# Optimization experiments

Hardware: AMD Instinct MI355X
Metric: run time of the kernel (lower is better)

Reference implementation:

```python
import jax, jax.numpy as jnp
import numpy as np

EPS_F = 1e-12
M, N = 64, 4096  # feature dim m, num nodes n


def setup_inputs() -> dict:
    key = jax.random.key(0)
    k1, k2, k3, k4 = jax.random.split(key, 4)
    # X: (m, n) node features transposed, as in the repo (features.t())
    X = jax.random.normal(k1, (M, N), dtype=jnp.float32)
    # F: (m, m) parameter, xavier_uniform init
    bound = float(np.sqrt(6.0 / (M + M)))
    F = jax.random.uniform(k2, (M, M), minval=-bound, maxval=bound, dtype=jnp.float32)
    # Q_S: (n, n) orthogonal eigenvector matrix of the (symmetric, normalized) adjacency
    A = jax.random.normal(k3, (N, N), dtype=jnp.float32)
    Q_S, _ = jnp.linalg.qr(A)
    Q_S = Q_S.astype(jnp.float32)
    # Lambda_S: (n, 1) eigenvalues of normalized adjacency, inside (-1, 1)
    Lambda_S = jnp.sort(
        jax.random.uniform(k4, (N, 1), minval=-0.95, maxval=0.95, dtype=jnp.float32), axis=0
    )
    gamma = jnp.asarray(0.8, dtype=jnp.float32)
    return {"X": X, "F": F, "Q_S": Q_S, "Lambda_S": Lambda_S, "gamma": gamma}


def reference(X, F, Q_S, Lambda_S, gamma):
    # g(F) = F^T F / (||F^T F||_F + eps)  -- Frobenius-normalized Gram matrix
    FF = F.T @ F                                   # (m, m)
    G_F = FF / (jnp.linalg.norm(FF) + EPS_F)       # (m, m), symmetric PSD, ||.||_F ~ 1
    # spectral decomposition of g(F)
    Lambda_F, Q_F = jnp.linalg.eigh(G_F)           # (m,), (m, m)
    # closed-form equilibrium of Z = gamma * g(F) Z S^T + X in the joint eigenbasis
    D = 1.0 / (1.0 - gamma * Lambda_F[:, None] * Lambda_S.reshape(1, -1))  # (m, n)
    Z = Q_F @ (D * (Q_F.T @ X @ Q_S)) @ Q_S.T      # (m, n)
    return Z
```

## Files before the change

### kernel.cpp

```cpp
#include <hip/hip_runtime.h>
#include <math.h>


typedef short short8 __attribute__((ext_vector_type(8)));
typedef float floatx16 __attribute__((ext_vector_type(16)));

#define KSPLIT 8
#define KCHUNK 512
constexpr int Mdim = 64;
constexpr int Ndim = 4096;

__device__ inline ushort f2bf(float f) {
    uint u = __float_as_uint(f);
    u += 0x7fff + ((u >> 16) & 1);
    return (ushort)(u >> 16);
}
__device__ inline float bf2f(ushort h) { return __uint_as_float(((uint)h) << 16); }

__device__ inline floatx16 mfma_bf16(short8 a, short8 b, floatx16 c) {
    return __builtin_amdgcn_mfma_f32_32x32x16_bf16(a, b, c, 0, 0, 0);
}

struct SharedGemm { ushort Ah[4096], Al[4096], Bh[4096], Bl[4096]; };
struct SharedPrep { float Fraw[64 * 65]; ushort Ph[4096], Pl[4096]; float red[256]; };
union SharedU { SharedGemm g; SharedPrep p; };

__global__ __launch_bounds__(256) void init_kernel(float* __restrict__ W, float* __restrict__ Z) {
    const int i = blockIdx.x * 256 + threadIdx.x;
    float4 z = {0.f, 0.f, 0.f, 0.f};
    if (i < 65536) *(float4*)&W[i * 4] = z;
    else *(float4*)&Z[(i - 65536) * 4] = z;
}

__device__ void prep_body(SharedPrep& sp, const float* __restrict__ F, float* __restrict__ Gout) {
    const int t = threadIdx.x;
    const int l = t & 63, w = t >> 6;
    const int tm = w & 1, tn = w >> 1;
    const int am = tm * 32 + (l & 31);
    const int bn = tn * 32 + (l & 31);
    const int lk = l >> 5;

    for (int s = 0; s < 4; ++s) {
        int e = t + 256 * s;
        int r = e >> 4, q = (e & 15) * 4;
        float4 v = *(const float4*)&F[r * 64 + q];
        float fa[4] = {v.x, v.y, v.z, v.w};
        for (int i = 0; i < 4; ++i) sp.Fraw[r * 65 + q + i] = fa[i];
    }
    __syncthreads();
    {
        int c = t >> 2, kbase = (t & 3) * 16;
        ushort hh[16], ll[16];
#pragma unroll
        for (int kk = 0; kk < 16; ++kk) {
            float v = sp.Fraw[(kbase + kk) * 65 + c];
            ushort h = f2bf(v);
            hh[kk] = h;
            ll[kk] = f2bf(v - bf2f(h));
        }
#pragma unroll
        for (int g = 0; g < 2; ++g) {
            int gk = (kbase >> 3) + g;
            int idx = c * 64 + ((gk ^ (c & 7)) * 8);
#pragma unroll
            for (int u = 0; u < 8; ++u) { sp.Ph[idx + u] = hh[8 * g + u]; sp.Pl[idx + u] = ll[8 * g + u]; }
        }
    }
    __syncthreads();
    floatx16 acc;
    for (int i = 0; i < 16; ++i) acc[i] = 0.f;
    for (int s16 = 0; s16 < 4; ++s16) {
        int gk = 2 * s16 + lk;
        int ai = am * 64 + ((gk ^ (am & 7)) * 8);
        int bi = bn * 64 + ((gk ^ (bn & 7)) * 8);
        short8 ah = *(const short8*)&sp.Ph[ai];
        short8 al = *(const short8*)&sp.Pl[ai];
        short8 bh = *(const short8*)&sp.Ph[bi];
        short8 bl = *(const short8*)&sp.Pl[bi];
        acc = mfma_bf16(ah, bh, acc);
        acc = mfma_bf16(al, bh, acc);
        acc = mfma_bf16(ah, bl, acc);
    }
    float ss = 0.f;
    for (int r = 0; r < 16; ++r) ss += acc[r] * acc[r];
    sp.red[t] = ss;
    __syncthreads();
    for (int off = 128; off > 0; off >>= 1) {
        if (t < off) sp.red[t] += sp.red[t + off];
        __syncthreads();
    }
    const float inv = 1.0f / (sqrtf(sp.red[0]) + 1e-12f);
    for (int r = 0; r < 16; ++r) {
        int row = (r & 3) + 8 * (r >> 2) + 4 * lk + tm * 32;
        int col = tn * 32 + (l & 31);
        float v = acc[r] * inv;
        Gout[row * 64 + col] = v;
        ushort h = f2bf(v);
        int idx = row * 64 + (((col >> 3) ^ (row & 7)) * 8 + (col & 7));
        sp.Ph[idx] = h;
        sp.Pl[idx] = f2bf(v - bf2f(h));
    }
    for (int j = 1; j < 5; ++j) {
        __syncthreads();
        floatx16 a2;
        for (int i = 0; i < 16; ++i) a2[i] = 0.f;
        for (int s16 = 0; s16 < 4; ++s16) {
            int gk = 2 * s16 + lk;
            int ai = am * 64 + ((gk ^ (am & 7)) * 8);
            int bi = bn * 64 + ((gk ^ (bn & 7)) * 8);
            short8 ah = *(const short8*)&sp.Ph[ai];
            short8 al = *(const short8*)&sp.Pl[ai];
            short8 bh = *(const short8*)&sp.Ph[bi];
            short8 bl = *(const short8*)&sp.Pl[bi];
            a2 = mfma_bf16(ah, bh, a2);
            a2 = mfma_bf16(al, bh, a2);
            a2 = mfma_bf16(ah, bl, a2);
        }
        __syncthreads();
        for (int r = 0; r < 16; ++r) {
            int row = (r & 3) + 8 * (r >> 2) + 4 * lk + tm * 32;
            int col = tn * 32 + (l & 31);
            float v = a2[r];
            Gout[j * 4096 + row * 64 + col] = v;
            ushort h = f2bf(v);
            int idx = row * 64 + (((col >> 3) ^ (row & 7)) * 8 + (col & 7));
            sp.Ph[idx] = h;
            sp.Pl[idx] = f2bf(v - bf2f(h));
        }
    }
}

template <bool TB, bool DOPREP>
__global__ __launch_bounds__(256, 4) void gemm_kernel(const float* __restrict__ A,
                                                      const float* __restrict__ Bm,
                                                      float* __restrict__ C,
                                                      const float* __restrict__ F,
                                                      float* __restrict__ Gp) {
    __shared__ SharedU sh;
    const int bid = blockIdx.x;
    if (DOPREP) {
        if (bid == 0) { prep_body(sh.p, F, Gp); return; }
    }
    const int b = DOPREP ? bid - 1 : bid;
    const int n0 = (b & 63) * 64;
    const int kb = (b >> 6) * KCHUNK;
    const int t = threadIdx.x;
    const int l = t & 63, w = t >> 6;
    const int tm = w & 1, tn = w >> 1;
    const int am = tm * 32 + (l & 31);
    const int bn = tn * 32 + (l & 31);
    const int lk = l >> 5;
    const int sr = t >> 2, sj = t & 3;
    const int nq = t & 15, kr2 = 2 * (t >> 4);

    floatx16 acc;
    for (int i = 0; i < 16; ++i) acc[i] = 0.f;

    for (int step = 0; step < KCHUNK / 64; ++step) {
        const int k0 = kb + step * 64;
        float4 av[4], bv[4], bva[2], bvb[2];
        for (int s = 0; s < 4; ++s)
            av[s] = *(const float4*)&A[sr * 4096 + k0 + 4 * sj + 16 * s];
        if (TB) {
            for (int s = 0; s < 4; ++s)
                bv[s] = *(const float4*)&Bm[(size_t)(n0 + sr) * 4096 + k0 + 4 * sj + 16 * s];
        } else {
            for (int s = 0; s < 2; ++s) {
                bva[s] = *(const float4*)&Bm[(size_t)(k0 + kr2 + 32 * s) * 4096 + n0 + 4 * nq];
                bvb[s] = *(const float4*)&Bm[(size_t)(k0 + kr2 + 1 + 32 * s) * 4096 + n0 + 4 * nq];
            }
        }
        __syncthreads();
        for (int s = 0; s < 4; ++s) {
            int off = 4 * sj + 16 * s;
            int idx = sr * 64 + (((off >> 3) ^ (sr & 7)) * 8 + (off & 7));
            float fa[4] = {av[s].x, av[s].y, av[s].z, av[s].w};
            ushort4 h4, l4;
            ushort* hp = (ushort*)&h4; ushort* lp = (ushort*)&l4;
            for (int i = 0; i < 4; ++i) {
                ushort h = f2bf(fa[i]);
                hp[i] = h; lp[i] = f2bf(fa[i] - bf2f(h));
            }
            *(ushort4*)&sh.g.Ah[idx] = h4;
            *(ushort4*)&sh.g.Al[idx] = l4;
        }
        if (TB) {
            for (int s = 0; s < 4; ++s) {
                int off = 4 * sj + 16 * s;
                int idx = sr * 64 + (((off >> 3) ^ (sr & 7)) * 8 + (off & 7));
                float fb[4] = {bv[s].x, bv[s].y, bv[s].z, bv[s].w};
                ushort4 h4, l4;
                ushort* hp = (ushort*)&h4; ushort* lp = (ushort*)&l4;
                for (int i = 0; i < 4; ++i) {
                    ushort h = f2bf(fb[i]);
                    hp[i] = h; lp[i] = f2bf(fb[i] - bf2f(h));
                }
                *(ushort4*)&sh.g.Bh[idx] = h4;
                *(ushort4*)&sh.g.Bl[idx] = l4;
            }
        } else {
            for (int s = 0; s < 2; ++s) {
                int k = kr2 + 32 * s;
                float fa[4] = {bva[s].x, bva[s].y, bva[s].z, bva[s].w};
                float fb[4] = {bvb[s].x, bvb[s].y, bvb[s].z, bvb[s].w};
                for (int i = 0; i < 4; ++i) {
                    int n = 4 * nq + i;
                    int idx = n * 64 + (((k >> 3) ^ (n & 7)) * 8 + (k & 7));
                    ushort2 hp2, lp2;
                    hp2.x = f2bf(fa[i]); hp2.y = f2bf(fb[i]);
                    lp2.x = f2bf(fa[i] - bf2f(hp2.x));
                    lp2.y = f2bf(fb[i] - bf2f(hp2.y));
                    *(ushort2*)&sh.g.Bh[idx] = hp2;
                    *(ushort2*)&sh.g.Bl[idx] = lp2;
                }
            }
        }
        __syncthreads();
#pragma unroll
        for (int s16 = 0; s16 < 4; ++s16) {
            int gk = 2 * s16 + lk;
            int ai = am * 64 + ((gk ^ (am & 7)) * 8);
            int bi = bn * 64 + ((gk ^ (bn & 7)) * 8);
            short8 ah = *(const short8*)&sh.g.Ah[ai];
            short8 al = *(const short8*)&sh.g.Al[ai];
            short8 bh = *(const short8*)&sh.g.Bh[bi];
            short8 bl = *(const short8*)&sh.g.Bl[bi];
            acc = mfma_bf16(ah, bh, acc);
            acc = mfma_bf16(al, bh, acc);
            acc = mfma_bf16(ah, bl, acc);
        }
    }
    const int colg = n0 + tn * 32 + (l & 31);
#pragma unroll
    for (int r = 0; r < 16; ++r) {
        int row = (r & 3) + 8 * (r >> 2) + 4 * lk + tm * 32;
        atomicAdd(&C[row * 4096 + colg], acc[r]);
    }
}

__global__ __launch_bounds__(256) void solve_kernel(const float* __restrict__ W,
                                                    const float* __restrict__ Gp,
                                                    const float* __restrict__ lam,
                                                    const float* __restrict__ gammap,
                                                    float* __restrict__ Y) {
    __shared__ float Gs[64][68];
    __shared__ float T[64][17];
    const int t = threadIdx.x;
    const int c0 = blockIdx.x * 16;
    for (int e = t; e < 1024; e += 256)
        T[e >> 4][e & 15] = W[(e >> 4) * 4096 + c0 + (e & 15)];
    const int tx = t & 15;
    const int r4 = (t >> 4) * 4;
    const float a = gammap[0] * lam[c0 + tx];
    float s = a;
    for (int j = 0; j < 5; ++j) {
        __syncthreads();
        for (int e = t; e < 4096; e += 256) Gs[e >> 6][e & 63] = Gp[j * 4096 + e];
        __syncthreads();
        float u0 = 0.f, u1 = 0.f, u2 = 0.f, u3 = 0.f;
#pragma unroll 8
        for (int k = 0; k < 64; ++k) {
            const float tv = T[k][tx];
            const float4 g = *(const float4*)&Gs[k][r4];
            u0 += g.x * tv; u1 += g.y * tv; u2 += g.z * tv; u3 += g.w * tv;
        }
        __syncthreads();
        T[r4 + 0][tx] += s * u0;
        T[r4 + 1][tx] += s * u1;
        T[r4 + 2][tx] += s * u2;
        T[r4 + 3][tx] += s * u3;
        s = s * s;
    }
    __syncthreads();
    for (int e = t; e < 1024; e += 256)
        Y[(e >> 4) * 4096 + c0 + (e & 15)] = T[e >> 4][e & 15];
}

extern "C" void kernel_launch(void* const* d_in, const int* in_sizes, int n_in,
                              void* d_out, int out_size, void* d_ws, size_t ws_size,
                              hipStream_t stream) {
    const float* X     = (const float*)d_in[0];
    const float* F     = (const float*)d_in[1];
    const float* Qs    = (const float*)d_in[2];
    const float* lam   = (const float*)d_in[3];
    const float* gamma = (const float*)d_in[4];
    float* Z = (float*)d_out;

    float* W  = (float*)d_ws;
    float* Y  = W + Mdim * Ndim;
    float* Gp = Y + Mdim * Ndim;

    init_kernel<<<512, 256, 0, stream>>>(W, Z);
    gemm_kernel<false, true><<<64 * KSPLIT + 1, 256, 0, stream>>>(X, Qs, W, F, Gp);
    solve_kernel<<<Ndim / 16, 256, 0, stream>>>(W, Gp, lam, gamma, Y);
    gemm_kernel<true, false><<<64 * KSPLIT, 256, 0, stream>>>(Y, Qs, Z, nullptr, nullptr);
}
```

Baseline: 169.2 us.

## Load GEMM operands directly into registers, drop LDS staging and low-part of Q

Both large GEMMs now load fragments straight from global memory into MFMA operand registers, removing shared-memory staging and the block barriers around it. The Q_S operand is kept only as a single bf16 high part, so each step issues two MFMAs instead of three. Conversions use packed bf16 intrinsics, and the K split is doubled to launch more blocks. In exchange, global loads are less coalesced (strided column reads for the first GEMM), precision drops slightly from ignoring Q's low bits, and twice as many atomic adds hit the output.

```diff
diff --git a/kernel.cpp b/kernel.cpp
--- a/kernel.cpp
+++ b/kernel.cpp
@@ -1,12 +1,13 @@
 #include <hip/hip_runtime.h>
+#include <hip/hip_bf16.h>
 #include <math.h>
 
 
 typedef short short8 __attribute__((ext_vector_type(8)));
 typedef float floatx16 __attribute__((ext_vector_type(16)));
 
-#define KSPLIT 8
-#define KCHUNK 512
+#define KSPLIT 16
+#define KCHUNK 256
 constexpr int Mdim = 64;
 constexpr int Ndim = 4096;
 
@@ -21,9 +22,23 @@
     return __builtin_amdgcn_mfma_f32_32x32x16_bf16(a, b, c, 0, 0, 0);
 }
 
-struct SharedGemm { ushort Ah[4096], Al[4096], Bh[4096], Bl[4096]; };
+union U8 { short8 v; ushort2 p[4]; };
+
+__device__ inline ushort2 pk_bf16(float a, float b) {
+    float2 f; f.x = a; f.y = b;
+    __hip_bfloat162 h = __float22bfloat162_rn(f);
+    return *(ushort2*)&h;
+}
+
+__device__ inline void split_pair(float f0, float f1, ushort2& h, ushort2& lo) {
+    h = pk_bf16(f0, f1);
+    uint hp = *(uint*)&h;
+    float g0 = __uint_as_float(hp << 16);
+    float g1 = __uint_as_float(hp & 0xffff0000u);
+    lo = pk_bf16(f0 - g0, f1 - g1);
+}
+
 struct SharedPrep { float Fraw[64 * 65]; ushort Ph[4096], Pl[4096]; float red[256]; };
-union SharedU { SharedGemm g; SharedPrep p; };
 
 __global__ __launch_bounds__(256) void init_kernel(float* __restrict__ W, float* __restrict__ Z) {
     const int i = blockIdx.x * 256 + threadIdx.x;
@@ -130,111 +145,95 @@
     }
 }
 
-template <bool TB, bool DOPREP>
-__global__ __launch_bounds__(256, 4) void gemm_kernel(const float* __restrict__ A,
-                                                      const float* __restrict__ Bm,
-                                                      float* __restrict__ C,
-                                                      const float* __restrict__ F,
-                                                      float* __restrict__ Gp) {
-    __shared__ SharedU sh;
+__global__ __launch_bounds__(256, 4) void gemm1_kernel(const float* __restrict__ X,
+                                                       const float* __restrict__ Qs,
+                                                       float* __restrict__ W,
+                                                       const float* __restrict__ F,
+                                                       float* __restrict__ Gp) {
+    __shared__ SharedPrep sp;
     const int bid = blockIdx.x;
-    if (DOPREP) {
-        if (bid == 0) { prep_body(sh.p, F, Gp); return; }
-    }
-    const int b = DOPREP ? bid - 1 : bid;
+    if (bid == 0) { prep_body(sp, F, Gp); return; }
+    const int b = bid - 1;
     const int n0 = (b & 63) * 64;
     const int kb = (b >> 6) * KCHUNK;
     const int t = threadIdx.x;
     const int l = t & 63, w = t >> 6;
     const int tm = w & 1, tn = w >> 1;
-    const int am = tm * 32 + (l & 31);
-    const int bn = tn * 32 + (l & 31);
-    const int lk = l >> 5;
-    const int sr = t >> 2, sj = t & 3;
-    const int nq = t & 15, kr2 = 2 * (t >> 4);
+    const int arow = tm * 32 + (l & 31);
+    const int bcol = n0 + tn * 32 + (l & 31);
+    const int lk8 = (l >> 5) * 8;
+    const float* Arow = X + (size_t)arow * 4096;
+    const float* Bcol = Qs + bcol;
 
     floatx16 acc;
     for (int i = 0; i < 16; ++i) acc[i] = 0.f;
 
-    for (int step = 0; step < KCHUNK / 64; ++step) {
-        const int k0 = kb + step * 64;
-        float4 av[4], bv[4], bva[2], bvb[2];
-        for (int s = 0; s < 4; ++s)
-            av[s] = *(const float4*)&A[sr * 4096 + k0 + 4 * sj + 16 * s];
-        if (TB) {
-            for (int s = 0; s < 4; ++s)
-                bv[s] = *(const float4*)&Bm[(size_t)(n0 + sr) * 4096 + k0 + 4 * sj + 16 * s];
-        } else {
-            for (int s = 0; s < 2; ++s) {
-                bva[s] = *(const float4*)&Bm[(size_t)(k0 + kr2 + 32 * s) * 4096 + n0 + 4 * nq];
-                bvb[s] = *(const float4*)&Bm[(size_t)(k0 + kr2 + 1 + 32 * s) * 4096 + n0 + 4 * nq];
-            }
-        }
-        __syncthreads();
-        for (int s = 0; s < 4; ++s) {
-            int off = 4 * sj + 16 * s;
-            int idx = sr * 64 + (((off >> 3) ^ (sr & 7)) * 8 + (off & 7));
-            float fa[4] = {av[s].x, av[s].y, av[s].z, av[s].w};
-            ushort4 h4, l4;
-            ushort* hp = (ushort*)&h4; ushort* lp = (ushort*)&l4;
-            for (int i = 0; i < 4; ++i) {
-                ushort h = f2bf(fa[i]);
-                hp[i] = h; lp[i] = f2bf(fa[i] - bf2f(h));
-            }
-            *(ushort4*)&sh.g.Ah[idx] = h4;
-            *(ushort4*)&sh.g.Al[idx] = l4;
-        }
-        if (TB) {
-            for (int s = 0; s < 4; ++s) {
-                int off = 4 * sj + 16 * s;
-                int idx = sr * 64 + (((off >> 3) ^ (sr & 7)) * 8 + (off & 7));
-                float fb[4] = {bv[s].x, bv[s].y, bv[s].z, bv[s].w};
-                ushort4 h4, l4;
-                ushort* hp = (ushort*)&h4; ushort* lp = (ushort*)&l4;
-                for (int i = 0; i < 4; ++i) {
-                    ushort h = f2bf(fb[i]);
-                    hp[i] = h; lp[i] = f2bf(fb[i] - bf2f(h));
-                }
-                *(ushort4*)&sh.g.Bh[idx] = h4;
-                *(ushort4*)&sh.g.Bl[idx] = l4;
-            }
-        } else {
-            for (int s = 0; s < 2; ++s) {
-                int k = kr2 + 32 * s;
-                float fa[4] = {bva[s].x, bva[s].y, bva[s].z, bva[s].w};
-                float fb[4] = {bvb[s].x, bvb[s].y, bvb[s].z, bvb[s].w};
-                for (int i = 0; i < 4; ++i) {
-                    int n = 4 * nq + i;
-                    int idx = n * 64 + (((k >> 3) ^ (n & 7)) * 8 + (k & 7));
-                    ushort2 hp2, lp2;
-                    hp2.x = f2bf(fa[i]); hp2.y = f2bf(fb[i]);
-                    lp2.x = f2bf(fa[i] - bf2f(hp2.x));
-                    lp2.y = f2bf(fb[i] - bf2f(hp2.y));
-                    *(ushort2*)&sh.g.Bh[idx] = hp2;
-                    *(ushort2*)&sh.g.Bl[idx] = lp2;
-                }
-            }
-        }
-        __syncthreads();
-#pragma unroll
-        for (int s16 = 0; s16 < 4; ++s16) {
-            int gk = 2 * s16 + lk;
-            int ai = am * 64 + ((gk ^ (am & 7)) * 8);
-            int bi = bn * 64 + ((gk ^ (bn & 7)) * 8);
-            short8 ah = *(const short8*)&sh.g.Ah[ai];
-            short8 al = *(const short8*)&sh.g.Al[ai];
-            short8 bh = *(const short8*)&sh.g.Bh[bi];
-            short8 bl = *(const short8*)&sh.g.Bl[bi];
-            acc = mfma_bf16(ah, bh, acc);
-            acc = mfma_bf16(al, bh, acc);
-            acc = mfma_bf16(ah, bl, acc);
-        }
-    }
-    const int colg = n0 + tn * 32 + (l & 31);
+#pragma unroll 2
+    for (int it = 0; it < KCHUNK / 16; ++it) {
+        const int k0 = kb + it * 16 + lk8;
+        float4 a0 = *(const float4*)&Arow[k0];
+        float4 a1 = *(const float4*)&Arow[k0 + 4];
+        float bw[8];
+#pragma unroll
+        for (int j = 0; j < 8; ++j) bw[j] = Bcol[(size_t)(k0 + j) * 4096];
+        U8 ah, al, bh;
+        split_pair(a0.x, a0.y, ah.p[0], al.p[0]);
+        split_pair(a0.z, a0.w, ah.p[1], al.p[1]);
+        split_pair(a1.x, a1.y, ah.p[2], al.p[2]);
+        split_pair(a1.z, a1.w, ah.p[3], al.p[3]);
+#pragma unroll
+        for (int j = 0; j < 4; ++j) bh.p[j] = pk_bf16(bw[2 * j], bw[2 * j + 1]);
+        acc = mfma_bf16(ah.v, bh.v, acc);
+        acc = mfma_bf16(al.v, bh.v, acc);
+    }
 #pragma unroll
     for (int r = 0; r < 16; ++r) {
-        int row = (r & 3) + 8 * (r >> 2) + 4 * lk + tm * 32;
-        atomicAdd(&C[row * 4096 + colg], acc[r]);
+        const int orow = (r & 3) + 8 * (r >> 2) + 4 * (l >> 5) + tm * 32;
+        atomicAdd(&W[orow * 4096 + bcol], acc[r]);
+    }
+}
+
+__global__ __launch_bounds__(256, 4) void gemm2_kernel(const float* __restrict__ Y,
+                                                       const float* __restrict__ Qs,
+                                                       float* __restrict__ Z) {
+    const int b = blockIdx.x;
+    const int n0 = (b & 63) * 64;
+    const int kb = (b >> 6) * KCHUNK;
+    const int t = threadIdx.x;
+    const int l = t & 63, w = t >> 6;
+    const int tm = w & 1, tn = w >> 1;
+    const int arow = tm * 32 + (l & 31);
+    const int bcol = n0 + tn * 32 + (l & 31);
+    const int lk8 = (l >> 5) * 8;
+    const float* Arow = Y + (size_t)arow * 4096;
+    const float* Brow = Qs + (size_t)bcol * 4096;
+
+    floatx16 acc;
+    for (int i = 0; i < 16; ++i) acc[i] = 0.f;
+
+#pragma unroll 2
+    for (int it = 0; it < KCHUNK / 16; ++it) {
+        const int k0 = kb + it * 16 + lk8;
+        float4 a0 = *(const float4*)&Arow[k0];
+        float4 a1 = *(const float4*)&Arow[k0 + 4];
+        float4 b0 = *(const float4*)&Brow[k0];
+        float4 b1 = *(const float4*)&Brow[k0 + 4];
+        U8 ah, al, bh;
+        split_pair(a0.x, a0.y, ah.p[0], al.p[0]);
+        split_pair(a0.z, a0.w, ah.p[1], al.p[1]);
+        split_pair(a1.x, a1.y, ah.p[2], al.p[2]);
+        split_pair(a1.z, a1.w, ah.p[3], al.p[3]);
+        bh.p[0] = pk_bf16(b0.x, b0.y);
+        bh.p[1] = pk_bf16(b0.z, b0.w);
+        bh.p[2] = pk_bf16(b1.x, b1.y);
+        bh.p[3] = pk_bf16(b1.z, b1.w);
+        acc = mfma_bf16(ah.v, bh.v, acc);
+        acc = mfma_bf16(al.v, bh.v, acc);
+    }
+#pragma unroll
+    for (int r = 0; r < 16; ++r) {
+        const int orow = (r & 3) + 8 * (r >> 2) + 4 * (l >> 5) + tm * 32;
+        atomicAdd(&Z[orow * 4096 + bcol], acc[r]);
     }
 }
 
@@ -291,7 +290,7 @@
     float* Gp = Y + Mdim * Ndim;
 
     init_kernel<<<512, 256, 0, stream>>>(W, Z);
-    gemm_kernel<false, true><<<64 * KSPLIT + 1, 256, 0, stream>>>(X, Qs, W, F, Gp);
+    gemm1_kernel<<<64 * KSPLIT + 1, 256, 0, stream>>>(X, Qs, W, F, Gp);
     solve_kernel<<<Ndim / 16, 256, 0, stream>>>(W, Gp, lam, gamma, Y);
-    gemm_kernel<true, false><<<64 * KSPLIT, 256, 0, stream>>>(Y, Qs, Z, nullptr, nullptr);
-}
+    gemm2_kernel<<<64 * KSPLIT, 256, 0, stream>>>(Y, Qs, Z);
+}
```

Result: slower. 175.8 us (+3.9%).
